# Performance work log

Hardware: AMD Instinct MI355X
Metric: run time of the kernel (lower is better)

The kernel has to match this reference:

```python
import jax, jax.numpy as jnp
import numpy as np

B, MBS, F, CD = 512, 32768, 512, 16  # batch, mini_batch_size, filter_length, cond_dim

def setup_inputs() -> dict:
    key = jax.random.key(0)
    ks = jax.random.split(key, 8)
    return {
        "inputs": jax.random.normal(ks[0], (B, MBS, 1), jnp.float32),
        "c": jax.random.normal(ks[1], (B, 1, CD), jnp.float32),
        "W0": jax.random.normal(ks[2], (CD, F), jnp.float32) * 0.1,
        "b0": jnp.zeros((F,), jnp.float32),
        "alpha": jnp.full((F,), 0.25, jnp.float32),
        "Wg": jax.random.normal(ks[3], (CD, F), jnp.float32) * 0.1,
        "bg": jnp.zeros((F,), jnp.float32),
        "Wb": jax.random.normal(ks[4], (CD, F), jnp.float32) * 0.1,
        "bb": jnp.zeros((F,), jnp.float32),
        "Wglu": jax.random.normal(ks[5], (F, 2 * F), jnp.float32) * 0.05,
        "bglu": jnp.zeros((2 * F,), jnp.float32),
        "Wf": jax.random.normal(ks[6], (F, F), jnp.float32) * 0.05,
        "bf": jnp.zeros((F,), jnp.float32),
    }

def reference(inputs, c, W0, b0, alpha, Wg, bg, Wb, bb, Wglu, bglu, Wf, bf):
    mbs = inputs.shape[1]
    flen = Wf.shape[1]
    # conditioning stack: Dense -> PReLU -> FiLM -> GLU -> Dense(softsign)
    c_ = c @ W0 + b0                                  # [B,1,F]
    c_ = jnp.where(c_ >= 0, c_, alpha * c_)           # PReLU
    c_ = c_ * (c @ Wg + bg) + (c @ Wb + bb)           # FiLM
    g = c_ @ Wglu + bglu                              # [B,1,2F]
    a, gate = jnp.split(g, 2, axis=-1)
    c_ = a * jax.nn.sigmoid(gate)                     # GLU
    filters = jax.nn.soft_sign(c_ @ Wf + bf)          # [B,1,F]
    # FFT-based circular (linear via zero pad) convolution
    conv_len = mbs + flen - 1
    X = jnp.fft.fft(inputs[:, :, 0].astype(jnp.complex64), n=conv_len)   # [B,conv_len]
    H = jnp.fft.fft(filters[:, 0, :].astype(jnp.complex64), n=conv_len)  # [B,conv_len]
    y = jnp.fft.ifft(X * H)
    return jnp.real(y[:, :mbs])                       # [B,MBS]
```

## Files before the change

kernel.cpp:

```cpp
#include <hip/hip_runtime.h>


typedef float f32x16 __attribute__((ext_vector_type(16)));
typedef float f32x4  __attribute__((ext_vector_type(4)));
typedef __bf16 bf16x8 __attribute__((ext_vector_type(8)));

__device__ __forceinline__ unsigned short f2bf(float f) {
    unsigned int u = __float_as_uint(f);
    u += 0x7FFFu + ((u >> 16) & 1u);
    return (unsigned short)(u >> 16);
}

__device__ __forceinline__ uint4 pack8n(float4 a, float4 b) {
    bf16x8 v;
    v[0] = (__bf16)a.x; v[1] = (__bf16)a.y; v[2] = (__bf16)a.z; v[3] = (__bf16)a.w;
    v[4] = (__bf16)b.x; v[5] = (__bf16)b.y; v[6] = (__bf16)b.z; v[7] = (__bf16)b.w;
    uint4 r;
    __builtin_memcpy(&r, &v, 16);
    return r;
}

__global__ __launch_bounds__(256) void kA(
    const float* __restrict__ Wglu, const float* __restrict__ Wf,
    const float* __restrict__ c, const float* __restrict__ W0,
    const float* __restrict__ b0, const float* __restrict__ alpha,
    const float* __restrict__ Wg, const float* __restrict__ bg,
    const float* __restrict__ Wb, const float* __restrict__ bb,
    unsigned short* __restrict__ WgluT, unsigned short* __restrict__ WfT,
    unsigned short* __restrict__ cfilm) {
    const int blk = blockIdx.x, tid = threadIdx.x;
    if (blk < 192) {
        __shared__ float ldsF[64 * 65];
        const float* src; unsigned short* dst; int tj, tk, srcld;
        if (blk < 128) { tj = blk >> 3; tk = blk & 7; src = Wglu; dst = WgluT; srcld = 1024; }
        else { int b2 = blk - 128; tj = b2 >> 3; tk = b2 & 7; src = Wf; dst = WfT; srcld = 512; }
#pragma unroll
        for (int rr = 0; rr < 16; ++rr) {
            int kl = (tid >> 6) + (rr << 2), jl = tid & 63;
            ldsF[kl * 65 + jl] = src[(size_t)(tk * 64 + kl) * srcld + tj * 64 + jl];
        }
        __syncthreads();
#pragma unroll
        for (int rr = 0; rr < 16; ++rr) {
            int jl = (tid >> 6) + (rr << 2), kl = tid & 63;
            dst[(size_t)(tj * 64 + jl) * 512 + tk * 64 + kl] = f2bf(ldsF[kl * 65 + jl]);
        }
    } else {
        int id = (blk - 192) * 256 + tid;
        int b = id >> 9, f = id & 511;
        const float* cb = c + b * 16;
        float d0 = 0.f, dg = 0.f, db = 0.f;
#pragma unroll
        for (int i = 0; i < 16; ++i) {
            float cv = cb[i];
            d0 += cv * W0[i * 512 + f];
            dg += cv * Wg[i * 512 + f];
            db += cv * Wb[i * 512 + f];
        }
        float pre = d0 + b0[f];
        float pr = pre >= 0.f ? pre : alpha[f] * pre;
        float v = pr * (dg + bg[f]) + (db + bb[f]);
        cfilm[id] = f2bf(v);
    }
}

__global__ __launch_bounds__(256) void k2_glu(
    const unsigned short* __restrict__ cfilm, const unsigned short* __restrict__ WgluT,
    const float* __restrict__ bglu, unsigned short* __restrict__ cglu) {
    int wid = (blockIdx.x * 256 + threadIdx.x) >> 6;
    int l = threadIdx.x & 63;
    int tm = wid >> 5, tn = wid & 31;
    int row = tm * 16 + (l & 15);
    int col = tn * 16 + (l & 15);
    int kh = 8 * (l >> 4);
    f32x4 accA, accG;
#pragma unroll
    for (int i = 0; i < 4; ++i) { accA[i] = 0.f; accG[i] = 0.f; }
    const unsigned short* ap  = cfilm + row * 512 + kh;
    const unsigned short* bap = WgluT + col * 512 + kh;
    const unsigned short* bgp = WgluT + (512 + col) * 512 + kh;
#pragma unroll
    for (int kc = 0; kc < 16; ++kc) {
        bf16x8 a   = *(const bf16x8*)(ap  + kc * 32);
        bf16x8 ba  = *(const bf16x8*)(bap + kc * 32);
        bf16x8 bgt = *(const bf16x8*)(bgp + kc * 32);
        accA = __builtin_amdgcn_mfma_f32_16x16x32_bf16(a, ba,  accA, 0, 0, 0);
        accG = __builtin_amdgcn_mfma_f32_16x16x32_bf16(a, bgt, accG, 0, 0, 0);
    }
    float biasA = bglu[col], biasG = bglu[512 + col];
#pragma unroll
    for (int r = 0; r < 4; ++r) {
        float ga = accA[r] + biasA;
        float gg = accG[r] + biasG;
        float s = 1.f / (1.f + expf(-gg));
        int m = (l >> 4) * 4 + r;
        cglu[(tm * 16 + m) * 512 + col] = f2bf(ga * s);
    }
}

__global__ __launch_bounds__(256) void k3_filt(
    const unsigned short* __restrict__ cglu, const unsigned short* __restrict__ WfT,
    const float* __restrict__ bfv, unsigned short* __restrict__ hout) {
    int wid = (blockIdx.x * 256 + threadIdx.x) >> 6;
    int l = threadIdx.x & 63;
    int tm = wid >> 5, tn = wid & 31;
    int row = tm * 16 + (l & 15);
    int col = tn * 16 + (l & 15);
    int kh = 8 * (l >> 4);
    f32x4 acc;
#pragma unroll
    for (int i = 0; i < 4; ++i) acc[i] = 0.f;
    const unsigned short* ap = cglu + row * 512 + kh;
    const unsigned short* bp = WfT + col * 512 + kh;
#pragma unroll
    for (int kc = 0; kc < 16; ++kc) {
        bf16x8 a  = *(const bf16x8*)(ap + kc * 32);
        bf16x8 bv = *(const bf16x8*)(bp + kc * 32);
        acc = __builtin_amdgcn_mfma_f32_16x16x32_bf16(a, bv, acc, 0, 0, 0);
    }
    float bias = bfv[col];
#pragma unroll
    for (int r = 0; r < 4; ++r) {
        float z = acc[r] + bias;
        float h = z / (1.f + fabsf(z));
        int m = (l >> 4) * 4 + r;
        hout[(tm * 16 + m) * 512 + col] = f2bf(h);
    }
}

__global__ __launch_bounds__(256, 2) void k5e(
    const float* __restrict__ x, const unsigned short* __restrict__ hbf,
    float* __restrict__ y) {
    __shared__ __align__(16) unsigned char smem[45184];
    const int tid = threadIdx.x;
    const int b = blockIdx.x;
    const float* xb = x + (size_t)b * 32768;
    unsigned short* hs = (unsigned short*)(smem + 44160);

    ((unsigned int*)hs)[tid] = ((const unsigned int*)(hbf + (size_t)b * 512))[tid];
    __syncthreads();

    for (int e = tid; e < 8 * 292; e += 256) {
        int s = e / 292, w2 = e - s * 292;
        int j0 = 2 * w2 + s;
        unsigned int v0 = (j0 >= 32 && j0 < 544) ? hs[543 - j0] : 0u;
        unsigned int v1 = (j0 >= 31 && j0 < 543) ? hs[542 - j0] : 0u;
        ((unsigned int*)(smem + 34816))[e] = v0 | (v1 << 16);
    }

#pragma unroll
    for (int r = 0; r < 5; ++r) {
        int slot = tid + (r << 8);
        if (slot < 1088) {
            int g = slot - 64;
            uint4 w4;
            if (g >= 0) {
                float4 a  = *(const float4*)(xb + g * 8);
                float4 b2 = *(const float4*)(xb + g * 8 + 4);
                w4 = pack8n(a, b2);
            } else {
                w4 = make_uint4(0u, 0u, 0u, 0u);
            }
            *(uint4*)(smem + ((slot ^ ((slot >> 3) & 7)) << 4)) = w4;
        }
    }
    __syncthreads();

    const int w = tid >> 6, l = tid & 63;
    const int q = l & 31, hl = l >> 5;
    const int lq = 4 * q + hl;
    const int abase = 66 + (w << 8) + lq;
    const int o0 = 559 - q + 8 * hl;
    const int s8 = o0 & 7;
    const unsigned char* hrb = smem + 34816 + s8 * 1168 + ((o0 - s8) << 1);

    for (int c = 0; c < 4; ++c) {
        const unsigned char* wb = smem + ((c & 1) ? 17408 : 0);
        unsigned char* sb = smem + ((c & 1) ? 0 : 17408);
        float4 La0, La1, La2, La3, La4, Lb0, Lb1, Lb2, Lb3, Lb4;
        if (c < 3) {
            const float* px = xb + (((c + 1) << 13) - 512);
            La0 = *(const float4*)(px + (tid << 3));           Lb0 = *(const float4*)(px + (tid << 3) + 4);
            La1 = *(const float4*)(px + ((tid + 256) << 3));   Lb1 = *(const float4*)(px + ((tid + 256) << 3) + 4);
            La2 = *(const float4*)(px + ((tid + 512) << 3));   Lb2 = *(const float4*)(px + ((tid + 512) << 3) + 4);
            La3 = *(const float4*)(px + ((tid + 768) << 3));   Lb3 = *(const float4*)(px + ((tid + 768) << 3) + 4);
            if (tid < 64) {
                La4 = *(const float4*)(px + ((tid + 1024) << 3));
                Lb4 = *(const float4*)(px + ((tid + 1024) << 3) + 4);
            }
        }
        f32x16 acc0, acc1;
#pragma unroll
        for (int i = 0; i < 16; ++i) { acc0[i] = 0.f; acc1[i] = 0.f; }
#pragma unroll
        for (int cc = 0; cc < 34; ++cc) {
            bf16x8 bfr = *(const bf16x8*)(hrb - (cc << 5));
            int a0 = abase - 2 * cc, a1 = a0 + 128;
            bf16x8 xa0 = *(const bf16x8*)(wb + ((a0 ^ ((a0 >> 3) & 7)) << 4));
            bf16x8 xa1 = *(const bf16x8*)(wb + ((a1 ^ ((a1 >> 3) & 7)) << 4));
            acc0 = __builtin_amdgcn_mfma_f32_32x32x16_bf16(xa0, bfr, acc0, 0, 0, 0);
            acc1 = __builtin_amdgcn_mfma_f32_32x32x16_bf16(xa1, bfr, acc1, 0, 0, 0);
        }
        if (c < 3) {
            int s0 = tid;
            *(uint4*)(sb + ((s0 ^ ((s0 >> 3) & 7)) << 4)) = pack8n(La0, Lb0);
            int s1 = tid + 256;
            *(uint4*)(sb + ((s1 ^ ((s1 >> 3) & 7)) << 4)) = pack8n(La1, Lb1);
            int s2 = tid + 512;
            *(uint4*)(sb + ((s2 ^ ((s2 >> 3) & 7)) << 4)) = pack8n(La2, Lb2);
            int s3 = tid + 768;
            *(uint4*)(sb + ((s3 ^ ((s3 >> 3) & 7)) << 4)) = pack8n(La3, Lb3);
            if (tid < 64) {
                int s4 = tid + 1024;
                *(uint4*)(sb + ((s4 ^ ((s4 >> 3) & 7)) << 4)) = pack8n(La4, Lb4);
            }
        }
        asm volatile("s_waitcnt lgkmcnt(0)" ::: "memory");
        __builtin_amdgcn_s_barrier();
        __builtin_amdgcn_sched_barrier(0);
        float* yb = y + (size_t)b * 32768 + (c << 13) + (w << 11) + q;
#pragma unroll
        for (int r = 0; r < 16; ++r) {
            int m = (r & 3) + 8 * (r >> 2) + 4 * hl;
            yb[m << 5] = acc0[r];
            yb[1024 + (m << 5)] = acc1[r];
        }
    }
}

extern "C" void kernel_launch(void* const* d_in, const int* in_sizes, int n_in,
                              void* d_out, int out_size, void* d_ws, size_t ws_size,
                              hipStream_t stream) {
    const float* x    = (const float*)d_in[0];
    const float* c    = (const float*)d_in[1];
    const float* W0   = (const float*)d_in[2];
    const float* b0   = (const float*)d_in[3];
    const float* al   = (const float*)d_in[4];
    const float* Wg   = (const float*)d_in[5];
    const float* bg   = (const float*)d_in[6];
    const float* Wb   = (const float*)d_in[7];
    const float* bb   = (const float*)d_in[8];
    const float* Wglu = (const float*)d_in[9];
    const float* bglu = (const float*)d_in[10];
    const float* Wf   = (const float*)d_in[11];
    const float* bf   = (const float*)d_in[12];
    float* y = (float*)d_out;

    char* ws = (char*)d_ws;
    unsigned short* cfilm = (unsigned short*)(ws);
    unsigned short* WgluT = (unsigned short*)(ws + 524288);
    unsigned short* WfT   = (unsigned short*)(ws + 1572864);
    unsigned short* cglu  = (unsigned short*)(ws + 2097152);
    unsigned short* hbf   = (unsigned short*)(ws + 2621440);

    kA<<<dim3(1216), dim3(256), 0, stream>>>(Wglu, Wf, c, W0, b0, al, Wg, bg, Wb, bb,
                                             WgluT, WfT, cfilm);
    k2_glu<<<dim3(256), dim3(256), 0, stream>>>(cfilm, WgluT, bglu, cglu);
    k3_filt<<<dim3(256), dim3(256), 0, stream>>>(cglu, WfT, bf, hbf);
    k5e<<<dim3(512), dim3(256), 0, stream>>>(x, hbf, y);
}
```

Baseline: 49.30 us.

## Fuse GLU and filter GEMM kernels into one kernel via LDS staging

Merges the GLU matmul and the softsign filter matmul into a single kernel. Each block handles one 16-row tile, keeps the GLU output in shared memory, and then computes the second GEMM from it. This removes a kernel launch and the global round trip of the intermediate. The trade-off is a grid of only 32 blocks of 512 threads, which leaves most CUs idle and gives each wave four times the serial work.

```diff
diff --git a/kernel.cpp b/kernel.cpp
--- a/kernel.cpp
+++ b/kernel.cpp
@@ -64,67 +64,65 @@
     }
 }
 
-__global__ __launch_bounds__(256) void k2_glu(
+__global__ __launch_bounds__(512) void k23(
     const unsigned short* __restrict__ cfilm, const unsigned short* __restrict__ WgluT,
-    const float* __restrict__ bglu, unsigned short* __restrict__ cglu) {
-    int wid = (blockIdx.x * 256 + threadIdx.x) >> 6;
-    int l = threadIdx.x & 63;
-    int tm = wid >> 5, tn = wid & 31;
-    int row = tm * 16 + (l & 15);
-    int col = tn * 16 + (l & 15);
-    int kh = 8 * (l >> 4);
-    f32x4 accA, accG;
-#pragma unroll
-    for (int i = 0; i < 4; ++i) { accA[i] = 0.f; accG[i] = 0.f; }
-    const unsigned short* ap  = cfilm + row * 512 + kh;
-    const unsigned short* bap = WgluT + col * 512 + kh;
-    const unsigned short* bgp = WgluT + (512 + col) * 512 + kh;
-#pragma unroll
-    for (int kc = 0; kc < 16; ++kc) {
-        bf16x8 a   = *(const bf16x8*)(ap  + kc * 32);
-        bf16x8 ba  = *(const bf16x8*)(bap + kc * 32);
-        bf16x8 bgt = *(const bf16x8*)(bgp + kc * 32);
-        accA = __builtin_amdgcn_mfma_f32_16x16x32_bf16(a, ba,  accA, 0, 0, 0);
-        accG = __builtin_amdgcn_mfma_f32_16x16x32_bf16(a, bgt, accG, 0, 0, 0);
-    }
-    float biasA = bglu[col], biasG = bglu[512 + col];
-#pragma unroll
-    for (int r = 0; r < 4; ++r) {
-        float ga = accA[r] + biasA;
-        float gg = accG[r] + biasG;
-        float s = 1.f / (1.f + expf(-gg));
-        int m = (l >> 4) * 4 + r;
-        cglu[(tm * 16 + m) * 512 + col] = f2bf(ga * s);
-    }
-}
-
-__global__ __launch_bounds__(256) void k3_filt(
-    const unsigned short* __restrict__ cglu, const unsigned short* __restrict__ WfT,
-    const float* __restrict__ bfv, unsigned short* __restrict__ hout) {
-    int wid = (blockIdx.x * 256 + threadIdx.x) >> 6;
-    int l = threadIdx.x & 63;
-    int tm = wid >> 5, tn = wid & 31;
-    int row = tm * 16 + (l & 15);
-    int col = tn * 16 + (l & 15);
-    int kh = 8 * (l >> 4);
-    f32x4 acc;
-#pragma unroll
-    for (int i = 0; i < 4; ++i) acc[i] = 0.f;
-    const unsigned short* ap = cglu + row * 512 + kh;
-    const unsigned short* bp = WfT + col * 512 + kh;
-#pragma unroll
-    for (int kc = 0; kc < 16; ++kc) {
-        bf16x8 a  = *(const bf16x8*)(ap + kc * 32);
-        bf16x8 bv = *(const bf16x8*)(bp + kc * 32);
-        acc = __builtin_amdgcn_mfma_f32_16x16x32_bf16(a, bv, acc, 0, 0, 0);
-    }
-    float bias = bfv[col];
-#pragma unroll
-    for (int r = 0; r < 4; ++r) {
-        float z = acc[r] + bias;
-        float h = z / (1.f + fabsf(z));
-        int m = (l >> 4) * 4 + r;
-        hout[(tm * 16 + m) * 512 + col] = f2bf(h);
+    const float* __restrict__ bglu, const unsigned short* __restrict__ WfT,
+    const float* __restrict__ bfv, unsigned short* __restrict__ hbf) {
+    __shared__ __align__(16) unsigned short cg[16][520];
+    const int tm = blockIdx.x;
+    const int w = threadIdx.x >> 6, l = threadIdx.x & 63;
+    const int lrow = l & 15, kh = 8 * (l >> 4);
+    const int row = tm * 16 + lrow;
+
+#pragma unroll
+    for (int j = 0; j < 4; ++j) {
+        int tn = w * 4 + j;
+        int col = tn * 16 + lrow;
+        f32x4 accA = {0.f, 0.f, 0.f, 0.f}, accG = {0.f, 0.f, 0.f, 0.f};
+        const unsigned short* ap  = cfilm + row * 512 + kh;
+        const unsigned short* bap = WgluT + (size_t)col * 512 + kh;
+        const unsigned short* bgp = WgluT + (size_t)(512 + col) * 512 + kh;
+#pragma unroll
+        for (int kc = 0; kc < 16; ++kc) {
+            bf16x8 a   = *(const bf16x8*)(ap  + kc * 32);
+            bf16x8 ba  = *(const bf16x8*)(bap + kc * 32);
+            bf16x8 bgt = *(const bf16x8*)(bgp + kc * 32);
+            accA = __builtin_amdgcn_mfma_f32_16x16x32_bf16(a, ba,  accA, 0, 0, 0);
+            accG = __builtin_amdgcn_mfma_f32_16x16x32_bf16(a, bgt, accG, 0, 0, 0);
+        }
+        float biasA = bglu[col], biasG = bglu[512 + col];
+#pragma unroll
+        for (int r = 0; r < 4; ++r) {
+            float ga = accA[r] + biasA;
+            float gg = accG[r] + biasG;
+            float s = 1.f / (1.f + expf(-gg));
+            int m = (l >> 4) * 4 + r;
+            cg[m][col] = f2bf(ga * s);
+        }
+    }
+    __syncthreads();
+
+#pragma unroll
+    for (int j = 0; j < 4; ++j) {
+        int tn = w * 4 + j;
+        int col = tn * 16 + lrow;
+        f32x4 acc = {0.f, 0.f, 0.f, 0.f};
+        const unsigned short* ap = &cg[lrow][kh];
+        const unsigned short* bp = WfT + (size_t)col * 512 + kh;
+#pragma unroll
+        for (int kc = 0; kc < 16; ++kc) {
+            bf16x8 a  = *(const bf16x8*)(ap + kc * 32);
+            bf16x8 bv = *(const bf16x8*)(bp + kc * 32);
+            acc = __builtin_amdgcn_mfma_f32_16x16x32_bf16(a, bv, acc, 0, 0, 0);
+        }
+        float bias = bfv[col];
+#pragma unroll
+        for (int r = 0; r < 4; ++r) {
+            float z = acc[r] + bias;
+            float h = z / (1.f + fabsf(z));
+            int m = (l >> 4) * 4 + r;
+            hbf[(size_t)(tm * 16 + m) * 512 + col] = f2bf(h);
+        }
     }
 }
 
@@ -250,12 +248,10 @@
     unsigned short* cfilm = (unsigned short*)(ws);
     unsigned short* WgluT = (unsigned short*)(ws + 524288);
     unsigned short* WfT   = (unsigned short*)(ws + 1572864);
-    unsigned short* cglu  = (unsigned short*)(ws + 2097152);
     unsigned short* hbf   = (unsigned short*)(ws + 2621440);
 
     kA<<<dim3(1216), dim3(256), 0, stream>>>(Wglu, Wf, c, W0, b0, al, Wg, bg, Wb, bb,
                                              WgluT, WfT, cfilm);
-    k2_glu<<<dim3(256), dim3(256), 0, stream>>>(cfilm, WgluT, bglu, cglu);
-    k3_filt<<<dim3(256), dim3(256), 0, stream>>>(cglu, WfT, bf, hbf);
+    k23<<<dim3(32), dim3(512), 0, stream>>>(cfilm, WgluT, bglu, WfT, bf, hbf);
     k5e<<<dim3(512), dim3(256), 0, stream>>>(x, hbf, y);
 }
```

Measured after the change: 94.02 us. +90.7%, slower.
